# Optimization experiments

Measured on AMD Instinct MI355X. Metric: run time of the kernel, lower is better.

Reference implementation:

```python
import jax, jax.numpy as jnp
import numpy as np

B, T, C = 2, 2048, 2048
NH, NKVH = 16, 4
HS = C // NH          # 128
KV = NKVH * HS        # 512
ROPE_BASE = 10000.0


def setup_inputs() -> dict:
    key = jax.random.key(0)
    k0, k1, k2 = jax.random.split(key, 3)
    x = jax.random.normal(k0, (B, T, C), dtype=jnp.float32)
    w_qkv = jax.random.normal(k1, (C, C + 2 * KV), dtype=jnp.float32) * 0.02
    b_qkv = jnp.zeros((C + 2 * KV,), dtype=jnp.float32)
    w_proj = jax.random.normal(k2, (C, C), dtype=jnp.float32) * 0.02
    b_proj = jnp.zeros((C,), dtype=jnp.float32)
    # RoPE frequencies: freqs_cis[t, j] = exp(i * t * base^(-2j/HS)), j in [0, HS/2)
    inv_freq = 1.0 / (ROPE_BASE ** (jnp.arange(0, HS, 2, dtype=jnp.float32) / HS))
    ang = jnp.arange(T, dtype=jnp.float32)[:, None] * inv_freq[None, :]  # [T, HS/2]
    return {
        "x": x, "w_qkv": w_qkv, "b_qkv": b_qkv,
        "w_proj": w_proj, "b_proj": b_proj,
        "freqs_cos": jnp.cos(ang), "freqs_sin": jnp.sin(ang),
    }


def _apply_rope(x, cos, sin):
    # x: [B, T, H, HS]; pairs (even, odd) along last dim are (real, imag)
    b, t, h, d = x.shape
    x_ = x.reshape(b, t, h, d // 2, 2)
    xr, xi = x_[..., 0], x_[..., 1]
    cos = cos[None, :, None, :]  # [1, T, 1, HS/2]
    sin = sin[None, :, None, :]
    out_r = xr * cos - xi * sin
    out_i = xr * sin + xi * cos
    return jnp.stack([out_r, out_i], axis=-1).reshape(b, t, h, d)


def reference(x, w_qkv, b_qkv, w_proj, b_proj, freqs_cos, freqs_sin):
    qkv = x @ w_qkv + b_qkv                      # [B, T, C + 2*KV]
    q, k, v = jnp.split(qkv, [C, C + KV], axis=2)
    q = q.reshape(B, T, NH, HS)
    k = k.reshape(B, T, NKVH, HS)
    v = v.reshape(B, T, NKVH, HS).transpose(0, 2, 1, 3)  # [B, NKVH, T, HS]
    q = _apply_rope(q, freqs_cos, freqs_sin)
    k = _apply_rope(k, freqs_cos, freqs_sin)
    q = q.transpose(0, 2, 1, 3)                  # [B, NH, T, HS]
    k = k.transpose(0, 2, 1, 3)                  # [B, NKVH, T, HS]
    kv_cache = (k, v)
    rep = NH // NKVH
    k_full = jnp.repeat(k, rep, axis=1)          # repeat_interleave on head dim
    v_full = jnp.repeat(v, rep, axis=1)
    scores = jnp.einsum("bhqd,bhkd->bhqk", q, k_full) / jnp.sqrt(jnp.float32(HS))
    causal = jnp.tril(jnp.ones((T, T), dtype=bool))
    scores = jnp.where(causal[None, None], scores, jnp.finfo(scores.dtype).min)
    attn = jax.nn.softmax(scores, axis=-1)
    y = jnp.einsum("bhqk,bhkd->bhqd", attn, v_full)
    y = y.transpose(0, 2, 1, 3).reshape(B, T, C)
    y = y @ w_proj + b_proj
    return y, kv_cache[0], kv_cache[1]
```

## Files before the change

### kernel.cpp

```cpp
#include <hip/hip_runtime.h>

typedef unsigned short u16;
typedef unsigned int u32;

#define B_    2
#define T_    2048
#define C_    2048
#define NH_   16
#define NKVH_ 4
#define HS_   128
#define NQKV  3072
#define M_    4096
#define SCALE 0.08838834764831845f
#define CC    0.12751742f
#define THR_RAW 62.0f

typedef __bf16 bf16x8 __attribute__((ext_vector_type(8)));
typedef float  f32x4  __attribute__((ext_vector_type(4)));
typedef float  f32x16 __attribute__((ext_vector_type(16)));
typedef unsigned int u32x2 __attribute__((ext_vector_type(2)));

__device__ __forceinline__ float bf2f(u16 u) {
    union { u32 i; float f; } x; x.i = ((u32)u) << 16; return x.f;
}
__device__ __forceinline__ u16 f2bf(float f) {
    union { float f; u32 i; } x; x.f = f;
    u32 r = x.i + 0x7fffu + ((x.i >> 16) & 1u);
    return (u16)(r >> 16);
}
__device__ __forceinline__ u32 cvtpk(float lo, float hi) {
    u32 r; asm("v_cvt_pk_bf16_f32 %0, %1, %2" : "=v"(r) : "v"(lo), "v"(hi));
    return r;
}

__device__ __forceinline__ void gload16(const void* g, void* l) {
    __builtin_amdgcn_global_load_lds(
        (const __attribute__((address_space(1))) u32*)g,
        (__attribute__((address_space(3))) u32*)l,
        16, 0, 0);
}

__global__ __launch_bounds__(256) void cast_f32_bf16(
    const float* __restrict__ in, u16* __restrict__ out, int n)
{
    int idx = (blockIdx.x * 256 + threadIdx.x) * 4;
    if (idx < n) {
        float4 v = *reinterpret_cast<const float4*>(in + idx);
        u32 p0 = (u32)f2bf(v.x) | ((u32)f2bf(v.y) << 16);
        u32 p1 = (u32)f2bf(v.z) | ((u32)f2bf(v.w) << 16);
        u32* o = (u32*)(out + idx);
        o[0] = p0; o[1] = p1;
    }
}

__global__ __launch_bounds__(256) void transpose_cast_f32_bf16(
    const float* __restrict__ in, u16* __restrict__ out, int R, int Cc)
{
    __shared__ float tile[32][33];
    int c0 = blockIdx.x * 32, r0 = blockIdx.y * 32;
    int tx = threadIdx.x & 31, ty = threadIdx.x >> 5;
#pragma unroll
    for (int i = 0; i < 4; ++i)
        tile[ty + i * 8][tx] = in[(size_t)(r0 + ty + i * 8) * Cc + c0 + tx];
    __syncthreads();
#pragma unroll
    for (int i = 0; i < 4; ++i)
        out[(size_t)(c0 + ty + i * 8) * R + r0 + tx] = f2bf(tile[tx][ty + i * 8]);
}

__global__ __launch_bounds__(256) void transpose_bf16_batched(
    const u16* __restrict__ in, u16* __restrict__ out, int R, int Cc)
{
    __shared__ u16 tile[32][33];
    int c0 = blockIdx.x * 32, r0 = blockIdx.y * 32;
    size_t zb = (size_t)blockIdx.z * R * Cc;
    int tx = threadIdx.x & 31, ty = threadIdx.x >> 5;
#pragma unroll
    for (int i = 0; i < 4; ++i)
        tile[ty + i * 8][tx] = in[zb + (size_t)(r0 + ty + i * 8) * Cc + c0 + tx];
    __syncthreads();
#pragma unroll
    for (int i = 0; i < 4; ++i)
        out[zb + (size_t)(c0 + ty + i * 8) * R + r0 + tx] = tile[tx][ty + i * 8];
}

template <int OUT_BF16>
__global__ __launch_bounds__(512, 2) void gemm8(
    const u16* __restrict__ A, const u16* __restrict__ Bt,
    const float* __restrict__ bias, void* __restrict__ Cv,
    int M, int N, int K)
{
    __shared__ __attribute__((aligned(16))) u16 As[2][2][8192];
    __shared__ __attribute__((aligned(16))) u16 Bs[2][2][8192];

    int tid = threadIdx.x, lane = tid & 63, w = tid >> 6;
    int l16 = lane & 15, hi = (lane >> 4) & 3;
    int wm = w >> 2, wn = w & 3;
    int brow = blockIdx.x * 256, bcol = blockIdx.y * 256;
    const int NT = K >> 6;

    f32x4 acc[8][4] = {};

    auto stageA = [&](int kt2, int kk, int buf) {
#pragma unroll
        for (int i = 0; i < 2; ++i) {
            u32 off = (u32)i * 8192 + (u32)w * 1024 + ((u32)lane << 4);
            u32 g = off ^ (((off >> 7) & 7) << 4);
            u32 r = g >> 6, s = (g >> 4) & 3;
            gload16(A + (size_t)(brow + r) * K + kt2 * 64 + kk * 32 + s * 8,
                    (char*)&As[buf][kk][0] + i * 8192 + w * 1024);
        }
    };
    auto stageB = [&](int kt2, int kk, int buf) {
#pragma unroll
        for (int i = 0; i < 2; ++i) {
            u32 off = (u32)i * 8192 + (u32)w * 1024 + ((u32)lane << 4);
            u32 g = off ^ (((off >> 7) & 7) << 4);
            u32 r = g >> 6, s = (g >> 4) & 3;
            gload16(Bt + (size_t)(bcol + r) * K + kt2 * 64 + kk * 32 + s * 8,
                    (char*)&Bs[buf][kk][0] + i * 8192 + w * 1024);
        }
    };

    stageA(0, 0, 0); stageB(0, 0, 0); stageA(0, 1, 0); stageB(0, 1, 0);
    if (NT > 1) {
        stageA(1, 0, 1); stageB(1, 0, 1); stageA(1, 1, 1);
        asm volatile("s_waitcnt vmcnt(6)" ::: "memory");
    } else {
        asm volatile("s_waitcnt vmcnt(0)" ::: "memory");
    }
    __builtin_amdgcn_s_barrier();

    for (int kt = 0; kt < NT; ++kt) {
        int cur = kt & 1, nxt = cur ^ 1;
        const char* Ak0 = (const char*)&As[cur][0][0];
        const char* Ak1 = (const char*)&As[cur][1][0];
        const char* Bk0 = (const char*)&Bs[cur][0][0];
        const char* Bk1 = (const char*)&Bs[cur][1][0];
        bf16x8 af[8], bf[2];

#pragma unroll
        for (int m = 0; m < 8; ++m) {
            u32 a = (u32)(wm * 128 + m * 16 + l16) * 64 + (u32)hi * 16;
            af[m] = *reinterpret_cast<const bf16x8*>(Ak0 + (a ^ (((a >> 7) & 7) << 4)));
        }
#pragma unroll
        for (int n = 0; n < 2; ++n) {
            u32 a = (u32)(wn * 64 + n * 16 + l16) * 64 + (u32)hi * 16;
            bf[n] = *reinterpret_cast<const bf16x8*>(Bk0 + (a ^ (((a >> 7) & 7) << 4)));
        }
        if (kt + 1 < NT) stageB(kt + 1, 1, nxt);
        __builtin_amdgcn_s_barrier();
        __builtin_amdgcn_s_setprio(1);
#pragma unroll
        for (int m = 0; m < 8; ++m) {
            acc[m][0] = __builtin_amdgcn_mfma_f32_16x16x32_bf16(af[m], bf[0], acc[m][0], 0, 0, 0);
            acc[m][1] = __builtin_amdgcn_mfma_f32_16x16x32_bf16(af[m], bf[1], acc[m][1], 0, 0, 0);
        }
        __builtin_amdgcn_s_setprio(0);
        __builtin_amdgcn_s_barrier();

#pragma unroll
        for (int n = 0; n < 2; ++n) {
            u32 a = (u32)(wn * 64 + 32 + n * 16 + l16) * 64 + (u32)hi * 16;
            bf[n] = *reinterpret_cast<const bf16x8*>(Bk0 + (a ^ (((a >> 7) & 7) << 4)));
        }
        if (kt + 2 < NT) stageA(kt + 2, 0, cur);
        __builtin_amdgcn_s_barrier();
        __builtin_amdgcn_s_setprio(1);
#pragma unroll
        for (int m = 0; m < 8; ++m) {
            acc[m][2] = __builtin_amdgcn_mfma_f32_16x16x32_bf16(af[m], bf[0], acc[m][2], 0, 0, 0);
            acc[m][3] = __builtin_amdgcn_mfma_f32_16x16x32_bf16(af[m], bf[1], acc[m][3], 0, 0, 0);
        }
        __builtin_amdgcn_s_setprio(0);
        __builtin_amdgcn_s_barrier();

#pragma unroll
        for (int m = 0; m < 8; ++m) {
            u32 a = (u32)(wm * 128 + m * 16 + l16) * 64 + (u32)hi * 16;
            af[m] = *reinterpret_cast<const bf16x8*>(Ak1 + (a ^ (((a >> 7) & 7) << 4)));
        }
#pragma unroll
        for (int n = 0; n < 2; ++n) {
            u32 a = (u32)(wn * 64 + n * 16 + l16) * 64 + (u32)hi * 16;
            bf[n] = *reinterpret_cast<const bf16x8*>(Bk1 + (a ^ (((a >> 7) & 7) << 4)));
        }
        if (kt + 2 < NT) stageB(kt + 2, 0, cur);
        __builtin_amdgcn_s_barrier();
        __builtin_amdgcn_s_setprio(1);
#pragma unroll
        for (int m = 0; m < 8; ++m) {
            acc[m][0] = __builtin_amdgcn_mfma_f32_16x16x32_bf16(af[m], bf[0], acc[m][0], 0, 0, 0);
            acc[m][1] = __builtin_amdgcn_mfma_f32_16x16x32_bf16(af[m], bf[1], acc[m][1], 0, 0, 0);
        }
        __builtin_amdgcn_s_setprio(0);
        __builtin_amdgcn_s_barrier();

#pragma unroll
        for (int n = 0; n < 2; ++n) {
            u32 a = (u32)(wn * 64 + 32 + n * 16 + l16) * 64 + (u32)hi * 16;
            bf[n] = *reinterpret_cast<const bf16x8*>(Bk1 + (a ^ (((a >> 7) & 7) << 4)));
        }
        if (kt + 2 < NT) stageA(kt + 2, 1, cur);
        __builtin_amdgcn_s_barrier();
        __builtin_amdgcn_s_setprio(1);
#pragma unroll
        for (int m = 0; m < 8; ++m) {
            acc[m][2] = __builtin_amdgcn_mfma_f32_16x16x32_bf16(af[m], bf[0], acc[m][2], 0, 0, 0);
            acc[m][3] = __builtin_amdgcn_mfma_f32_16x16x32_bf16(af[m], bf[1], acc[m][3], 0, 0, 0);
        }
        __builtin_amdgcn_s_setprio(0);
        if (kt + 1 < NT) {
            if (kt + 2 < NT) asm volatile("s_waitcnt vmcnt(6)" ::: "memory");
            else             asm volatile("s_waitcnt vmcnt(0)" ::: "memory");
        }
        __builtin_amdgcn_s_barrier();
    }

#pragma unroll
    for (int n = 0; n < 4; ++n) {
        int col = bcol + wn * 64 + n * 16 + l16;
        float bv = bias[col];
#pragma unroll
        for (int m = 0; m < 8; ++m) {
#pragma unroll
            for (int j = 0; j < 4; ++j) {
                int row = brow + wm * 128 + m * 16 + hi * 4 + j;
                float v = acc[m][n][j] + bv;
                if (OUT_BF16)
                    ((u16*)Cv)[(size_t)row * N + col] = f2bf(v);
                else
                    ((float*)Cv)[(size_t)row * N + col] = v;
            }
        }
    }
}

__global__ __launch_bounds__(256) void rope_scatter(
    const u16* __restrict__ qkv,
    const float* __restrict__ fcos, const float* __restrict__ fsin,
    u16* __restrict__ qb, u16* __restrict__ kb, u16* __restrict__ vb,
    float* __restrict__ kc, float* __restrict__ vc)
{
    int bt = blockIdx.x;
    int b = bt >> 11, t = bt & 2047;
    const u16* row = qkv + (size_t)bt * NQKV;
    for (int s = threadIdx.x; s < NQKV / 2; s += 256) {
        int col = s * 2;
        if (col < C_) {
            int h = col >> 7, d = col & 127;
            float xr = bf2f(row[col]), xi = bf2f(row[col + 1]);
            int fi = t * 64 + (d >> 1);
            float c = fcos[fi], sn = fsin[fi];
            size_t o = ((size_t)(b * NH_ + h) * T_ + t) * HS_ + d;
            qb[o]     = f2bf(xr * c - xi * sn);
            qb[o + 1] = f2bf(xr * sn + xi * c);
        } else if (col < C_ + NKVH_ * HS_) {
            int cc = col - C_;
            int h = cc >> 7, d = cc & 127;
            float xr = bf2f(row[col]), xi = bf2f(row[col + 1]);
            int fi = t * 64 + (d >> 1);
            float c = fcos[fi], sn = fsin[fi];
            float yr = xr * c - xi * sn, yi = xr * sn + xi * c;
            size_t o = ((size_t)(b * NKVH_ + h) * T_ + t) * HS_ + d;
            kb[o] = f2bf(yr); kb[o + 1] = f2bf(yi);
            kc[o] = yr;       kc[o + 1] = yi;
        } else {
            int cc = col - (C_ + NKVH_ * HS_);
            int h = cc >> 7, d = cc & 127;
            float v0 = bf2f(row[col]), v1 = bf2f(row[col + 1]);
            size_t o = ((size_t)(b * NKVH_ + h) * T_ + t) * HS_ + d;
            vb[o] = f2bf(v0); vb[o + 1] = f2bf(v1);
            vc[o] = v0;       vc[o + 1] = v1;
        }
    }
}

#define STAGE_KV(it_, buf_)                                               \
  {                                                                       \
    int _it = (it_);                                                      \
    _Pragma("unroll")                                                     \
    for (int i = 0; i < 4; ++i) {                                         \
      int chunk = w * 4 + i;                                              \
      int rk = chunk * 4 + (lane >> 4);                                   \
      int ck = ((lane & 15) ^ (rk & 7)) << 3;                             \
      gload16(Kp + (size_t)(_it * 64 + rk) * HS_ + ck,                    \
              (char*)Ks[buf_] + chunk * 1024);                            \
      int rv = chunk * 8 + (lane >> 3);                                   \
      int cv = ((lane & 7) ^ (rv & 7)) << 3;                              \
      gload16(Vp + (size_t)rv * T_ + _it * 64 + cv,                       \
              (char*)Vs[buf_] + chunk * 1024);                            \
    }                                                                     \
  }

__global__ __launch_bounds__(256, 2) void attn_kernel(
    const u16* __restrict__ qb,
    const u16* __restrict__ kb,
    const u16* __restrict__ vt,
    u16* __restrict__ aout)
{
    __shared__ __attribute__((aligned(16))) u16 Ks[2][64 * 128];
    __shared__ __attribute__((aligned(16))) u16 Vs[2][128 * 64];

    int xx = blockIdx.x, yy = blockIdx.y;
    int qt = (yy < 16) ? (15 - xx) : xx;
    int bh = yy, b = bh >> 4, h = bh & 15, kvh = h >> 2;
    int lane = threadIdx.x & 63, w = threadIdx.x >> 6;
    int l32 = lane & 31, l5 = lane >> 5;
    int xorm = (l32 & 7) << 3;
    int koff = 8 * l5;

    const u16* Qp = qb + ((size_t)(b * NH_ + h) * T_ + qt * 128 + w * 32) * HS_;
    const u16* Kp = kb + (size_t)(b * NKVH_ + kvh) * T_ * HS_;
    const u16* Vp = vt + (size_t)(b * NKVH_ + kvh) * HS_ * T_;

    bf16x8 qf[8];
#pragma unroll
    for (int kd = 0; kd < 8; ++kd)
        qf[kd] = *reinterpret_cast<const bf16x8*>(
            Qp + (size_t)l32 * HS_ + kd * 16 + koff);

    f32x16 o[4] = {};
    float m = -1e30f, lrow = 0.f;
    int qg = qt * 128 + w * 32 + l32;
    int qmaxw = qt * 128 + w * 32 + 31;

    int ntiles = 2 * qt + 2;
    STAGE_KV(0, 0);

    for (int it = 0; it < ntiles; ++it) {
        int buf = it & 1;
        __syncthreads();
        if (it + 1 < ntiles) STAGE_KV(it + 1, buf ^ 1);

        if (it * 64 <= qmaxw) {
            const u16* Kbase = Ks[buf];
            const u16* Vbase = Vs[buf];

            f32x16 sacc[2] = {};
#pragma unroll
            for (int kt2 = 0; kt2 < 2; ++kt2)
#pragma unroll
                for (int kd = 0; kd < 8; ++kd) {
                    bf16x8 kf = *reinterpret_cast<const bf16x8*>(
                        Kbase + (kt2 * 32 + l32) * 128 + ((kd * 16 + koff) ^ xorm));
                    sacc[kt2] = __builtin_amdgcn_mfma_f32_32x32x16_bf16(
                        kf, qf[kd], sacc[kt2], 0, 0, 0);
                }

            if (it * 64 + 63 > qt * 128 + w * 32) {
#pragma unroll
                for (int kt2 = 0; kt2 < 2; ++kt2)
#pragma unroll
                    for (int r = 0; r < 16; ++r) {
                        int kvg = it * 64 + kt2 * 32 + (r & 3) + 8 * (r >> 2) + 4 * l5;
                        if (kvg > qg) sacc[kt2][r] = -1e30f;
                    }
            }

            float mx;
            {
                float t8[8];
#pragma unroll
                for (int i = 0; i < 8; ++i) {
                    float a = fmaxf(sacc[0][i], sacc[0][i + 8]);
                    float c = fmaxf(sacc[1][i], sacc[1][i + 8]);
                    t8[i] = fmaxf(a, c);
                }
                float t4a = fmaxf(t8[0], t8[1]), t4b = fmaxf(t8[2], t8[3]);
                float t4c = fmaxf(t8[4], t8[5]), t4d = fmaxf(t8[6], t8[7]);
                mx = fmaxf(fmaxf(t4a, t4b), fmaxf(t4c, t4d));
                mx = fmaxf(mx, __shfl_xor(mx, 32));
            }

            if (!__all(mx <= m + THR_RAW)) {
                float nm = fmaxf(m, mx);
                float al = exp2f(CC * (m - nm));
                m = nm;
                lrow *= al;
#pragma unroll
                for (int r = 0; r < 16; ++r) {
                    float af = __shfl(al, (r & 3) + 8 * (r >> 2) + 4 * l5, 64);
                    o[0][r] *= af; o[1][r] *= af; o[2][r] *= af; o[3][r] *= af;
                }
            }
            float mcm = -CC * m;

            f32x16 p[2];
#pragma unroll
            for (int kt2 = 0; kt2 < 2; ++kt2)
#pragma unroll
                for (int r = 0; r < 16; ++r)
                    p[kt2][r] = exp2f(__builtin_fmaf(CC, sacc[kt2][r], mcm));
            {
                float s8[8];
#pragma unroll
                for (int i = 0; i < 8; ++i)
                    s8[i] = (p[0][i] + p[0][i + 8]) + (p[1][i] + p[1][i + 8]);
                float s4a = s8[0] + s8[1], s4b = s8[2] + s8[3];
                float s4c = s8[4] + s8[5], s4d = s8[6] + s8[7];
                float rs = (s4a + s4b) + (s4c + s4d);
                rs += __shfl_xor(rs, 32);
                lrow += rs;
            }

#pragma unroll
            for (int ks = 0; ks < 4; ++ks) {
                int e = ks & 1, kh = ks >> 1;
                u32 a0 = cvtpk(p[kh][8 * e + 0], p[kh][8 * e + 1]);
                u32 a1 = cvtpk(p[kh][8 * e + 2], p[kh][8 * e + 3]);
                u32 b0 = cvtpk(p[kh][8 * e + 4], p[kh][8 * e + 5]);
                u32 b1 = cvtpk(p[kh][8 * e + 6], p[kh][8 * e + 7]);
                u32x2 s0 = __builtin_amdgcn_permlane32_swap(a0, b0, false, false);
                u32x2 s1 = __builtin_amdgcn_permlane32_swap(a1, b1, false, false);
                union { u32 u[4]; bf16x8 v; } pu;
                pu.u[0] = s0[0]; pu.u[1] = s1[0]; pu.u[2] = s0[1]; pu.u[3] = s1[1];
                bf16x8 pf = pu.v;
#pragma unroll
                for (int dt = 0; dt < 4; ++dt) {
                    bf16x8 vf = *reinterpret_cast<const bf16x8*>(
                        Vbase + (dt * 32 + l32) * 64 + ((ks * 16 + koff) ^ xorm));
                    o[dt] = __builtin_amdgcn_mfma_f32_32x32x16_bf16(
                        pf, vf, o[dt], 0, 0, 0);
                }
            }
        }
    }

    float inv = 1.0f / lrow;
#pragma unroll
    for (int r = 0; r < 16; ++r) {
        int ql = (r & 3) + 8 * (r >> 2) + 4 * l5;
        float iv = __shfl(inv, ql, 64);
        int trow = qt * 128 + w * 32 + ql;
        size_t base = ((size_t)b * T_ + trow) * C_ + h * HS_ + l32;
#pragma unroll
        for (int dt = 0; dt < 4; ++dt)
            aout[base + dt * 32] = f2bf(o[dt][r] * iv);
    }
}

extern "C" void kernel_launch(void* const* d_in, const int* in_sizes, int n_in,
                              void* d_out, int out_size, void* d_ws, size_t ws_size,
                              hipStream_t stream)
{
    const float* x      = (const float*)d_in[0];
    const float* w_qkv  = (const float*)d_in[1];
    const float* b_qkv  = (const float*)d_in[2];
    const float* w_proj = (const float*)d_in[3];
    const float* b_proj = (const float*)d_in[4];
    const float* fcos   = (const float*)d_in[5];
    const float* fsin   = (const float*)d_in[6];

    float* y  = (float*)d_out;
    float* kc = y + (size_t)B_ * T_ * C_;
    float* vc = kc + (size_t)B_ * NKVH_ * T_ * HS_;

    char* ws = (char*)d_ws;
    u16* xb     = (u16*)(ws);
    u16* wprojT = (u16*)(ws);
    u16* wqkvT = (u16*)(ws + 16777216);
    u16* kbuf  = (u16*)(ws + 16777216);
    u16* vbuf  = (u16*)(ws + 16777216 + 4194304);
    u16* vtb   = (u16*)(ws + 16777216 + 8388608);
    u16* qkv  = (u16*)(ws + 29360128);
    u16* aout = (u16*)(ws + 29360128);
    u16* qbuf = (u16*)(ws + 54525952);

    cast_f32_bf16<<<M_ * C_ / 1024, 256, 0, stream>>>(x, xb, M_ * C_);
    transpose_cast_f32_bf16<<<dim3(NQKV / 32, C_ / 32), 256, 0, stream>>>(
        w_qkv, wqkvT, C_, NQKV);
    gemm8<1><<<dim3(M_ / 256, NQKV / 256), 512, 0, stream>>>(
        xb, wqkvT, b_qkv, qkv, M_, NQKV, C_);
    rope_scatter<<<M_, 256, 0, stream>>>(qkv, fcos, fsin, qbuf, kbuf, vbuf, kc, vc);
    transpose_bf16_batched<<<dim3(HS_ / 32, T_ / 32, B_ * NKVH_), 256, 0, stream>>>(
        vbuf, vtb, T_, HS_);
    transpose_cast_f32_bf16<<<dim3(C_ / 32, C_ / 32), 256, 0, stream>>>(
        w_proj, wprojT, C_, C_);
    attn_kernel<<<dim3(T_ / 128, B_ * NH_), 256, 0, stream>>>(qbuf, kbuf, vtb, aout);
    gemm8<0><<<dim3(M_ / 256, C_ / 256), 512, 0, stream>>>(
        aout, wprojT, b_proj, y, M_, C_, C_);
}
```

Before: 238.5 us.

## Template GEMM M-tile, remap workgroups for XCD locality, restructure fragment loads

The GEMM is templated on the number of M fragments, so the output projection runs with 128x256 tiles and twice as many workgroups. Workgroup IDs are remapped so consecutive IDs spread across the 8 XCDs, which is meant to improve L2 locality. The inner loop now loads all four B fragments at once and splits A into halves, which changes register pressure and LDS read ordering. The attention kernel also raises wave priority around its MFMA blocks. The smaller tile lowers per-block data reuse and the remap assumes the workgroup count divides by 8.

```diff
diff --git a/kernel.cpp b/kernel.cpp
--- a/kernel.cpp
+++ b/kernel.cpp
@@ -84,26 +84,33 @@
         out[zb + (size_t)(c0 + ty + i * 8) * R + r0 + tx] = tile[tx][ty + i * 8];
 }
 
-template <int OUT_BF16>
+template <int MFRAG, int OUT_BF16>
 __global__ __launch_bounds__(512, 2) void gemm8(
     const u16* __restrict__ A, const u16* __restrict__ Bt,
     const float* __restrict__ bias, void* __restrict__ Cv,
     int M, int N, int K)
 {
-    __shared__ __attribute__((aligned(16))) u16 As[2][2][8192];
+    constexpr int MH = MFRAG / 2;
+    constexpr int LA = MFRAG / 4;
+    constexpr int ASZ = MFRAG * 1024;
+    __shared__ __attribute__((aligned(16))) u16 As[2][2][ASZ];
     __shared__ __attribute__((aligned(16))) u16 Bs[2][2][8192];
 
     int tid = threadIdx.x, lane = tid & 63, w = tid >> 6;
     int l16 = lane & 15, hi = (lane >> 4) & 3;
     int wm = w >> 2, wn = w & 3;
-    int brow = blockIdx.x * 256, bcol = blockIdx.y * 256;
+
+    int gx = gridDim.x, nwg = gx * gridDim.y;
+    int id = blockIdx.y * gx + blockIdx.x;
+    int nid = (id & 7) * (nwg >> 3) + (id >> 3);
+    int brow = (nid % gx) * (MFRAG * 32), bcol = (nid / gx) * 256;
+
     const int NT = K >> 6;
-
-    f32x4 acc[8][4] = {};
+    f32x4 acc[MFRAG][4] = {};
 
     auto stageA = [&](int kt2, int kk, int buf) {
 #pragma unroll
-        for (int i = 0; i < 2; ++i) {
+        for (int i = 0; i < LA; ++i) {
             u32 off = (u32)i * 8192 + (u32)w * 1024 + ((u32)lane << 4);
             u32 g = off ^ (((off >> 7) & 7) << 4);
             u32 r = g >> 6, s = (g >> 4) & 3;
@@ -121,11 +128,28 @@
                     (char*)&Bs[buf][kk][0] + i * 8192 + w * 1024);
         }
     };
+    auto readA = [&](const u16* base, int mh, bf16x8* dst) {
+#pragma unroll
+        for (int m = 0; m < MH; ++m) {
+            u32 a = (u32)((wm * MFRAG + mh * MH + m) * 16 + l16) * 64 + (u32)hi * 16;
+            dst[m] = *reinterpret_cast<const bf16x8*>(
+                (const char*)base + (a ^ (((a >> 7) & 7) << 4)));
+        }
+    };
+    auto readB = [&](const u16* base, bf16x8* dst) {
+#pragma unroll
+        for (int n = 0; n < 4; ++n) {
+            u32 a = (u32)(wn * 64 + n * 16 + l16) * 64 + (u32)hi * 16;
+            dst[n] = *reinterpret_cast<const bf16x8*>(
+                (const char*)base + (a ^ (((a >> 7) & 7) << 4)));
+        }
+    };
 
     stageA(0, 0, 0); stageB(0, 0, 0); stageA(0, 1, 0); stageB(0, 1, 0);
     if (NT > 1) {
         stageA(1, 0, 1); stageB(1, 0, 1); stageA(1, 1, 1);
-        asm volatile("s_waitcnt vmcnt(6)" ::: "memory");
+        if constexpr (MFRAG == 8) asm volatile("s_waitcnt vmcnt(6)" ::: "memory");
+        else                      asm volatile("s_waitcnt vmcnt(4)" ::: "memory");
     } else {
         asm volatile("s_waitcnt vmcnt(0)" ::: "memory");
     }
@@ -133,87 +157,68 @@
 
     for (int kt = 0; kt < NT; ++kt) {
         int cur = kt & 1, nxt = cur ^ 1;
-        const char* Ak0 = (const char*)&As[cur][0][0];
-        const char* Ak1 = (const char*)&As[cur][1][0];
-        const char* Bk0 = (const char*)&Bs[cur][0][0];
-        const char* Bk1 = (const char*)&Bs[cur][1][0];
-        bf16x8 af[8], bf[2];
-
-#pragma unroll
-        for (int m = 0; m < 8; ++m) {
-            u32 a = (u32)(wm * 128 + m * 16 + l16) * 64 + (u32)hi * 16;
-            af[m] = *reinterpret_cast<const bf16x8*>(Ak0 + (a ^ (((a >> 7) & 7) << 4)));
-        }
-#pragma unroll
-        for (int n = 0; n < 2; ++n) {
-            u32 a = (u32)(wn * 64 + n * 16 + l16) * 64 + (u32)hi * 16;
-            bf[n] = *reinterpret_cast<const bf16x8*>(Bk0 + (a ^ (((a >> 7) & 7) << 4)));
-        }
+        const u16* Ac0 = &As[cur][0][0];
+        const u16* Ac1 = &As[cur][1][0];
+        const u16* Bc0 = &Bs[cur][0][0];
+        const u16* Bc1 = &Bs[cur][1][0];
+        bf16x8 af0[MH], af1[MH], af2[MH], af3[MH], bf0[4], bf1[4];
+
+        readA(Ac0, 0, af0); readB(Bc0, bf0); readA(Ac0, 1, af1);
         if (kt + 1 < NT) stageB(kt + 1, 1, nxt);
         __builtin_amdgcn_s_barrier();
         __builtin_amdgcn_s_setprio(1);
 #pragma unroll
-        for (int m = 0; m < 8; ++m) {
-            acc[m][0] = __builtin_amdgcn_mfma_f32_16x16x32_bf16(af[m], bf[0], acc[m][0], 0, 0, 0);
-            acc[m][1] = __builtin_amdgcn_mfma_f32_16x16x32_bf16(af[m], bf[1], acc[m][1], 0, 0, 0);
-        }
+        for (int m = 0; m < MH; ++m)
+#pragma unroll
+            for (int n = 0; n < 4; ++n)
+                acc[m][n] = __builtin_amdgcn_mfma_f32_16x16x32_bf16(
+                    af0[m], bf0[n], acc[m][n], 0, 0, 0);
         __builtin_amdgcn_s_setprio(0);
         __builtin_amdgcn_s_barrier();
 
-#pragma unroll
-        for (int n = 0; n < 2; ++n) {
-            u32 a = (u32)(wn * 64 + 32 + n * 16 + l16) * 64 + (u32)hi * 16;
-            bf[n] = *reinterpret_cast<const bf16x8*>(Bk0 + (a ^ (((a >> 7) & 7) << 4)));
-        }
+        readA(Ac1, 0, af2); readB(Bc1, bf1);
         if (kt + 2 < NT) stageA(kt + 2, 0, cur);
         __builtin_amdgcn_s_barrier();
         __builtin_amdgcn_s_setprio(1);
 #pragma unroll
-        for (int m = 0; m < 8; ++m) {
-            acc[m][2] = __builtin_amdgcn_mfma_f32_16x16x32_bf16(af[m], bf[0], acc[m][2], 0, 0, 0);
-            acc[m][3] = __builtin_amdgcn_mfma_f32_16x16x32_bf16(af[m], bf[1], acc[m][3], 0, 0, 0);
-        }
+        for (int m = 0; m < MH; ++m)
+#pragma unroll
+            for (int n = 0; n < 4; ++n)
+                acc[MH + m][n] = __builtin_amdgcn_mfma_f32_16x16x32_bf16(
+                    af1[m], bf0[n], acc[MH + m][n], 0, 0, 0);
         __builtin_amdgcn_s_setprio(0);
         __builtin_amdgcn_s_barrier();
 
-#pragma unroll
-        for (int m = 0; m < 8; ++m) {
-            u32 a = (u32)(wm * 128 + m * 16 + l16) * 64 + (u32)hi * 16;
-            af[m] = *reinterpret_cast<const bf16x8*>(Ak1 + (a ^ (((a >> 7) & 7) << 4)));
-        }
-#pragma unroll
-        for (int n = 0; n < 2; ++n) {
-            u32 a = (u32)(wn * 64 + n * 16 + l16) * 64 + (u32)hi * 16;
-            bf[n] = *reinterpret_cast<const bf16x8*>(Bk1 + (a ^ (((a >> 7) & 7) << 4)));
-        }
+        readA(Ac1, 1, af3);
         if (kt + 2 < NT) stageB(kt + 2, 0, cur);
         __builtin_amdgcn_s_barrier();
         __builtin_amdgcn_s_setprio(1);
 #pragma unroll
-        for (int m = 0; m < 8; ++m) {
-            acc[m][0] = __builtin_amdgcn_mfma_f32_16x16x32_bf16(af[m], bf[0], acc[m][0], 0, 0, 0);
-            acc[m][1] = __builtin_amdgcn_mfma_f32_16x16x32_bf16(af[m], bf[1], acc[m][1], 0, 0, 0);
-        }
+        for (int m = 0; m < MH; ++m)
+#pragma unroll
+            for (int n = 0; n < 4; ++n)
+                acc[m][n] = __builtin_amdgcn_mfma_f32_16x16x32_bf16(
+                    af2[m], bf1[n], acc[m][n], 0, 0, 0);
         __builtin_amdgcn_s_setprio(0);
         __builtin_amdgcn_s_barrier();
 
-#pragma unroll
-        for (int n = 0; n < 2; ++n) {
-            u32 a = (u32)(wn * 64 + 32 + n * 16 + l16) * 64 + (u32)hi * 16;
-            bf[n] = *reinterpret_cast<const bf16x8*>(Bk1 + (a ^ (((a >> 7) & 7) << 4)));
-        }
         if (kt + 2 < NT) stageA(kt + 2, 1, cur);
         __builtin_amdgcn_s_barrier();
         __builtin_amdgcn_s_setprio(1);
 #pragma unroll
-        for (int m = 0; m < 8; ++m) {
-            acc[m][2] = __builtin_amdgcn_mfma_f32_16x16x32_bf16(af[m], bf[0], acc[m][2], 0, 0, 0);
-            acc[m][3] = __builtin_amdgcn_mfma_f32_16x16x32_bf16(af[m], bf[1], acc[m][3], 0, 0, 0);
-        }
+        for (int m = 0; m < MH; ++m)
+#pragma unroll
+            for (int n = 0; n < 4; ++n)
+                acc[MH + m][n] = __builtin_amdgcn_mfma_f32_16x16x32_bf16(
+                    af3[m], bf1[n], acc[MH + m][n], 0, 0, 0);
         __builtin_amdgcn_s_setprio(0);
         if (kt + 1 < NT) {
-            if (kt + 2 < NT) asm volatile("s_waitcnt vmcnt(6)" ::: "memory");
-            else             asm volatile("s_waitcnt vmcnt(0)" ::: "memory");
+            if (kt + 2 < NT) {
+                if constexpr (MFRAG == 8) asm volatile("s_waitcnt vmcnt(6)" ::: "memory");
+                else                      asm volatile("s_waitcnt vmcnt(4)" ::: "memory");
+            } else {
+                asm volatile("s_waitcnt vmcnt(0)" ::: "memory");
+            }
         }
         __builtin_amdgcn_s_barrier();
     }
@@ -223,10 +228,10 @@
         int col = bcol + wn * 64 + n * 16 + l16;
         float bv = bias[col];
 #pragma unroll
-        for (int m = 0; m < 8; ++m) {
+        for (int m = 0; m < MFRAG; ++m) {
 #pragma unroll
             for (int j = 0; j < 4; ++j) {
-                int row = brow + wm * 128 + m * 16 + hi * 4 + j;
+                int row = brow + wm * (MFRAG * 16) + m * 16 + hi * 4 + j;
                 float v = acc[m][n][j] + bv;
                 if (OUT_BF16)
                     ((u16*)Cv)[(size_t)row * N + col] = f2bf(v);
@@ -339,6 +344,7 @@
             const u16* Vbase = Vs[buf];
 
             f32x16 sacc[2] = {};
+            __builtin_amdgcn_s_setprio(1);
 #pragma unroll
             for (int kt2 = 0; kt2 < 2; ++kt2)
 #pragma unroll
@@ -348,6 +354,7 @@
                     sacc[kt2] = __builtin_amdgcn_mfma_f32_32x32x16_bf16(
                         kf, qf[kd], sacc[kt2], 0, 0, 0);
                 }
+            __builtin_amdgcn_s_setprio(0);
 
             if (it * 64 + 63 > qt * 128 + w * 32) {
 #pragma unroll
@@ -405,6 +412,7 @@
                 lrow += rs;
             }
 
+            __builtin_amdgcn_s_setprio(1);
 #pragma unroll
             for (int ks = 0; ks < 4; ++ks) {
                 int e = ks & 1, kh = ks >> 1;
@@ -425,6 +433,7 @@
                         pf, vf, o[dt], 0, 0, 0);
                 }
             }
+            __builtin_amdgcn_s_setprio(0);
         }
     }
 
@@ -471,7 +480,7 @@
     cast_f32_bf16<<<M_ * C_ / 1024, 256, 0, stream>>>(x, xb, M_ * C_);
     transpose_cast_f32_bf16<<<dim3(NQKV / 32, C_ / 32), 256, 0, stream>>>(
         w_qkv, wqkvT, C_, NQKV);
-    gemm8<1><<<dim3(M_ / 256, NQKV / 256), 512, 0, stream>>>(
+    gemm8<8, 1><<<dim3(M_ / 256, NQKV / 256), 512, 0, stream>>>(
         xb, wqkvT, b_qkv, qkv, M_, NQKV, C_);
     rope_scatter<<<M_, 256, 0, stream>>>(qkv, fcos, fsin, qbuf, kbuf, vbuf, kc, vc);
     transpose_bf16_batched<<<dim3(HS_ / 32, T_ / 32, B_ * NKVH_), 256, 0, stream>>>(
@@ -479,6 +488,6 @@
     transpose_cast_f32_bf16<<<dim3(C_ / 32, C_ / 32), 256, 0, stream>>>(
         w_proj, wprojT, C_, C_);
     attn_kernel<<<dim3(T_ / 128, B_ * NH_), 256, 0, stream>>>(qbuf, kbuf, vtb, aout);
-    gemm8<0><<<dim3(M_ / 256, C_ / 256), 512, 0, stream>>>(
+    gemm8<4, 0><<<dim3(M_ / 128, C_ / 256), 512, 0, stream>>>(
         aout, wprojT, b_proj, y, M_, C_, C_);
 }
```

Measured after the change: 233.6 us. 2.1% less time.
